# Performance work log

Measured on AMD Instinct MI355X. Metric: run time of the kernel, lower is better.

## Reference

```python
import jax, jax.numpy as jnp
import numpy as np

NUM_HEADS = 8
NUM_LAYERS = 4
ATTN_DIM = 256
INPUT_DIM = 256
HEAD_DIM = ATTN_DIM // NUM_HEADS


def setup_inputs() -> dict:
    key = jax.random.key(0)
    ks = jax.random.split(key, 4)
    B, N = 32, 512
    agents_state = jax.random.normal(ks[0], (B, N, INPUT_DIM), dtype=jnp.float32)
    # normc_initializer(0.01): small std weights; bias zeros (torch default bias is
    # uniform but zeros suffice for a baseline; kept as explicit params)
    Wq = jax.random.normal(ks[1], (ATTN_DIM, INPUT_DIM), dtype=jnp.float32) * 0.01
    Wk = jax.random.normal(ks[2], (ATTN_DIM, INPUT_DIM), dtype=jnp.float32) * 0.01
    Wv = jax.random.normal(ks[3], (ATTN_DIM, INPUT_DIM), dtype=jnp.float32) * 0.01
    bq = jnp.zeros((ATTN_DIM,), dtype=jnp.float32)
    bk = jnp.zeros((ATTN_DIM,), dtype=jnp.float32)
    bv = jnp.zeros((ATTN_DIM,), dtype=jnp.float32)
    return {"agents_state": agents_state, "Wq": Wq, "bq": bq, "Wk": Wk, "bk": bk, "Wv": Wv, "bv": bv}


def _mha(q, k, v):
    # q: [B, N, D]; k, v: [B, M, D]
    B, N, _ = q.shape
    M = k.shape[1]
    qh = q.reshape(B, N, NUM_HEADS, HEAD_DIM)
    kh = k.reshape(B, M, NUM_HEADS, HEAD_DIM)
    vh = v.reshape(B, M, NUM_HEADS, HEAD_DIM)
    scores = jnp.einsum('bnhd,bmhd->bnhm', qh, kh) / np.float32(HEAD_DIM ** 0.5)
    attn = jax.nn.softmax(scores, axis=-1)
    out = jnp.einsum('bnhm,bmhd->bnhd', attn, vh)
    return out.reshape(B, N, ATTN_DIM)


def reference(agents_state, Wq, bq, Wk, bk, Wv, bv):
    queries = agents_state @ Wq.T + bq
    keys = agents_state @ Wk.T + bk
    values = agents_state @ Wv.T + bv
    attn_output = queries
    for _ in range(NUM_LAYERS):
        attn_output = attn_output + _mha(attn_output, keys, values)
    return attn_output
```

## Files before the change

kernel.cpp:

```cpp
#include <hip/hip_runtime.h>

typedef __bf16 bf16x8 __attribute__((ext_vector_type(8)));
typedef float  f32x4  __attribute__((ext_vector_type(4)));

#define K_SCALE 0.25505402682247326f

static __device__ __forceinline__ unsigned short f2bf(float f) {
  return __builtin_bit_cast(unsigned short, (__bf16)f);
}
static __device__ __forceinline__ f32x4 mfma16(bf16x8 a, bf16x8 b, f32x4 c) {
  return __builtin_amdgcn_mfma_f32_16x16x32_bf16(a, b, c, 0, 0, 0);
}

__global__ __launch_bounds__(256) void prep_kernel(
    const float* __restrict__ Wq, const float* __restrict__ bq,
    const float* __restrict__ Wk, const float* __restrict__ bk,
    const float* __restrict__ Wv, const float* __restrict__ bv,
    unsigned short* __restrict__ Wf, float* __restrict__ bias) {
  if (blockIdx.x == 96) {
    int t = threadIdx.x;
#pragma unroll
    for (int kseg = 0; kseg < 3; ++kseg) {
      int i = kseg * 256 + t;
      float bb;
      if (i < 256)      bb = bq[i];
      else if (i < 512) bb = bk[i - 256] * K_SCALE;
      else              bb = bv[i - 512];
      bias[i] = bb;
    }
    return;
  }
  int fidx = blockIdx.x * 256 + threadIdx.x;
  int lane = fidx & 63;
  int ks = (fidx >> 6) & 7;
  int ct = fidx >> 9;
  int n = ct * 16 + (lane & 15);
  int kk = ks * 32 + (lane >> 4) * 8;
  const float* src;
  float scale = 1.0f;
  if (n < 256)      src = Wq + n * 256 + kk;
  else if (n < 512) { src = Wk + (n - 256) * 256 + kk; scale = K_SCALE; }
  else              src = Wv + (n - 512) * 256 + kk;
  float4 f0 = reinterpret_cast<const float4*>(src)[0];
  float4 f1 = reinterpret_cast<const float4*>(src)[1];
  bf16x8 h;
  h[0] = (__bf16)(f0.x * scale); h[1] = (__bf16)(f0.y * scale);
  h[2] = (__bf16)(f0.z * scale); h[3] = (__bf16)(f0.w * scale);
  h[4] = (__bf16)(f1.x * scale); h[5] = (__bf16)(f1.y * scale);
  h[6] = (__bf16)(f1.z * scale); h[7] = (__bf16)(f1.w * scale);
  *reinterpret_cast<bf16x8*>(Wf + fidx * 8) = h;
}

__global__ __launch_bounds__(512, 4) void qkv_kernel(
    const float* __restrict__ X, const unsigned short* __restrict__ Wf,
    const float* __restrict__ bias, float* __restrict__ Qout,
    unsigned short* __restrict__ Kb, unsigned short* __restrict__ Vt) {
  __shared__ __align__(16) unsigned short Alds[32 * 256];
  const int tid = threadIdx.x;
  const int rowbase = blockIdx.x * 32;
  {
    int idx = tid * 16;
    int r = idx >> 8, k = idx & 255;
    const float4* src = reinterpret_cast<const float4*>(X + (rowbase + r) * 256 + k);
    float4 f0 = src[0], f1 = src[1], f2 = src[2], f3 = src[3];
    bf16x8 h0, h1;
    h0[0]=(__bf16)f0.x; h0[1]=(__bf16)f0.y; h0[2]=(__bf16)f0.z; h0[3]=(__bf16)f0.w;
    h0[4]=(__bf16)f1.x; h0[5]=(__bf16)f1.y; h0[6]=(__bf16)f1.z; h0[7]=(__bf16)f1.w;
    h1[0]=(__bf16)f2.x; h1[1]=(__bf16)f2.y; h1[2]=(__bf16)f2.z; h1[3]=(__bf16)f2.w;
    h1[4]=(__bf16)f3.x; h1[5]=(__bf16)f3.y; h1[6]=(__bf16)f3.z; h1[7]=(__bf16)f3.w;
    int c0 = k >> 3;
    int p0 = (c0 & 24) | ((c0 ^ r) & 7);
    int p1 = ((c0 + 1) & 24) | (((c0 + 1) ^ r) & 7);
    *reinterpret_cast<bf16x8*>(&Alds[r * 256 + p0 * 8]) = h0;
    *reinterpret_cast<bf16x8*>(&Alds[r * 256 + p1 * 8]) = h1;
  }
  __syncthreads();
  const int w = tid >> 6, lane = tid & 63, c = lane & 15, quad = lane >> 4;
  const f32x4 zf = {0.f, 0.f, 0.f, 0.f};
  for (int p = 0; p < 6; ++p) {
    int ct = w * 6 + p;
    f32x4 acc[2] = {zf, zf};
#pragma unroll
    for (int ks = 0; ks < 8; ++ks) {
      bf16x8 bf = *reinterpret_cast<const bf16x8*>(Wf + ((ct * 8 + ks) * 64 + lane) * 8);
#pragma unroll
      for (int mg = 0; mg < 2; ++mg) {
        int m = mg * 16 + c;
        int c8 = ks * 4 + quad;
        int ph = (c8 & 24) | ((c8 ^ m) & 7);
        bf16x8 af = *reinterpret_cast<const bf16x8*>(&Alds[m * 256 + ph * 8]);
        acc[mg] = mfma16(af, bf, acc[mg]);
      }
    }
    int col = ct * 16 + c;
    float bb = bias[col];
#pragma unroll
    for (int mg = 0; mg < 2; ++mg) {
      int growb = rowbase + mg * 16 + quad * 4;
      int b = growb >> 9, nrow = growb & 511;
      if (col < 256) {
#pragma unroll
        for (int r = 0; r < 4; ++r)
          Qout[(growb + r) * 256 + col] = acc[mg][r] + bb;
      } else if (col < 512) {
        int d = col & 31, hh = (col - 256) >> 5;
        int pd = ((d >> 2) & 3) * 8 + ((d >> 4) & 1) * 4 + (d & 3);
#pragma unroll
        for (int r = 0; r < 4; ++r)
          Kb[((b * 8 + hh) * 512 + nrow + r) * 32 + pd] = f2bf(acc[mg][r] + bb);
      } else {
        int d = col & 31, hh = (col - 512) >> 5;
        int pnb = (nrow & ~31) + ((nrow >> 2) & 3) * 8 + ((nrow >> 4) & 1) * 4;
        ushort4 pk;
        pk.x = f2bf(acc[mg][0] + bb); pk.y = f2bf(acc[mg][1] + bb);
        pk.z = f2bf(acc[mg][2] + bb); pk.w = f2bf(acc[mg][3] + bb);
        *reinterpret_cast<ushort4*>(&Vt[((b * 8 + hh) * 32 + d) * 512 + pnb]) = pk;
      }
    }
  }
}

__global__ __launch_bounds__(512, 4) void attn_kernel(
    const float* Q0, const unsigned short* __restrict__ Kg,
    const unsigned short* __restrict__ Vg, float* Out) {
  __shared__ __align__(16) unsigned short Ks[16384];
  __shared__ __align__(16) unsigned short Vts[16384];
  const int tid = threadIdx.x;
  const int bh = blockIdx.x >> 1, seg = blockIdx.x & 1;
  const int b = bh >> 3, h = bh & 7;
  const unsigned short* kgp = Kg + bh * 16384;
  const unsigned short* vgp = Vg + bh * 16384;
#pragma unroll
  for (int it = 0; it < 4; ++it) {
    int idx = it * 4096 + tid * 8;
    {
      int n = idx >> 5, g = (idx >> 3) & 3;
      bf16x8 v = *reinterpret_cast<const bf16x8*>(kgp + idx);
      *reinterpret_cast<bf16x8*>(&Ks[n * 32 + ((g ^ ((n >> 1) & 3)) << 3)]) = v;
    }
    {
      int d = idx >> 9, nn = idx & 511;
      bf16x8 v = *reinterpret_cast<const bf16x8*>(vgp + idx);
      int g = (nn >> 3) ^ (d & 7);
      *reinterpret_cast<bf16x8*>(&Vts[d * 512 + g * 8]) = v;
    }
  }
  const int w = tid >> 6, lane = tid & 63, c = lane & 15, quad = lane >> 4;
  const int rowq = seg * 256 + w * 32;
  f32x4 x[2][2];
#pragma unroll
  for (int rg = 0; rg < 2; ++rg)
#pragma unroll
    for (int tt = 0; tt < 2; ++tt)
      x[rg][tt] = *reinterpret_cast<const f32x4*>(
          Q0 + (b * 512 + rowq + rg * 16 + c) * 256 + h * 32 + tt * 16 + quad * 4);
  __syncthreads();
  const f32x4 zf = {0.f, 0.f, 0.f, 0.f};
  bf16x8 ones;
#pragma unroll
  for (int j = 0; j < 8; ++j) ones[j] = (__bf16)1.0f;
#pragma unroll 1
  for (int layer = 0; layer < 4; ++layer) {
    bf16x8 aq[2];
#pragma unroll
    for (int rg = 0; rg < 2; ++rg) {
      aq[rg][0] = (__bf16)x[rg][0][0]; aq[rg][1] = (__bf16)x[rg][0][1];
      aq[rg][2] = (__bf16)x[rg][0][2]; aq[rg][3] = (__bf16)x[rg][0][3];
      aq[rg][4] = (__bf16)x[rg][1][0]; aq[rg][5] = (__bf16)x[rg][1][1];
      aq[rg][6] = (__bf16)x[rg][1][2]; aq[rg][7] = (__bf16)x[rg][1][3];
    }
    f32x4 sacc[2] = {zf, zf};
    f32x4 O[2][2] = {{zf, zf}, {zf, zf}};
#pragma unroll 4
    for (int ch = 0; ch < 16; ++ch) {
      f32x4 S[2][2];
#pragma unroll
      for (int tt = 0; tt < 2; ++tt) {
        int n = (ch * 2 + tt) * 16 + c;
        bf16x8 kf = *reinterpret_cast<const bf16x8*>(
            &Ks[n * 32 + ((quad ^ ((c >> 1) & 3)) << 3)]);
#pragma unroll
        for (int rg = 0; rg < 2; ++rg) S[rg][tt] = mfma16(kf, aq[rg], zf);
      }
      bf16x8 ap[2];
#pragma unroll
      for (int rg = 0; rg < 2; ++rg) {
#pragma unroll
        for (int tt = 0; tt < 2; ++tt)
#pragma unroll
          for (int r = 0; r < 4; ++r)
            S[rg][tt][r] = __builtin_amdgcn_exp2f(S[rg][tt][r]);
        ap[rg][0] = (__bf16)S[rg][0][0]; ap[rg][1] = (__bf16)S[rg][0][1];
        ap[rg][2] = (__bf16)S[rg][0][2]; ap[rg][3] = (__bf16)S[rg][0][3];
        ap[rg][4] = (__bf16)S[rg][1][0]; ap[rg][5] = (__bf16)S[rg][1][1];
        ap[rg][6] = (__bf16)S[rg][1][2]; ap[rg][7] = (__bf16)S[rg][1][3];
        sacc[rg] = mfma16(ones, ap[rg], sacc[rg]);
      }
#pragma unroll
      for (int tt = 0; tt < 2; ++tt) {
        int d = tt * 16 + c;
        int gv = (ch * 4 + quad) ^ (c & 7);
        bf16x8 vf = *reinterpret_cast<const bf16x8*>(&Vts[d * 512 + gv * 8]);
#pragma unroll
        for (int rg = 0; rg < 2; ++rg) O[rg][tt] = mfma16(vf, ap[rg], O[rg][tt]);
      }
    }
#pragma unroll
    for (int rg = 0; rg < 2; ++rg) {
      float inv = __builtin_amdgcn_rcpf(sacc[rg][0]);
#pragma unroll
      for (int tt = 0; tt < 2; ++tt)
#pragma unroll
        for (int r = 0; r < 4; ++r) x[rg][tt][r] += O[rg][tt][r] * inv;
    }
  }
#pragma unroll
  for (int rg = 0; rg < 2; ++rg)
#pragma unroll
    for (int tt = 0; tt < 2; ++tt)
      *reinterpret_cast<f32x4*>(
          Out + (b * 512 + rowq + rg * 16 + c) * 256 + h * 32 + tt * 16 + quad * 4) = x[rg][tt];
}

extern "C" void kernel_launch(void* const* d_in, const int* in_sizes, int n_in,
                              void* d_out, int out_size, void* d_ws, size_t ws_size,
                              hipStream_t stream) {
  const float* X  = (const float*)d_in[0];
  const float* Wq = (const float*)d_in[1];
  const float* bq = (const float*)d_in[2];
  const float* Wk = (const float*)d_in[3];
  const float* bk = (const float*)d_in[4];
  const float* Wv = (const float*)d_in[5];
  const float* bv = (const float*)d_in[6];
  char* ws = (char*)d_ws;
  unsigned short* Wf   = (unsigned short*)(ws);
  float*          bias = (float*)(ws + 393216);
  unsigned short* Kb   = (unsigned short*)(ws + 397312);
  unsigned short* Vt   = (unsigned short*)(ws + 397312 + 8388608);
  float* out = (float*)d_out;
  prep_kernel<<<97, 256, 0, stream>>>(Wq, bq, Wk, bk, Wv, bv, Wf, bias);
  qkv_kernel<<<512, 512, 0, stream>>>(X, Wf, bias, out, Kb, Vt);
  attn_kernel<<<512, 512, 0, stream>>>(out, Kb, Vt, out);
}
```

Measured before the change: 132.8 us.

## Read K/V fragments directly from global memory instead of staging in LDS

The attention kernel no longer copies each head's K and V into shared memory. Each wave now loads its MFMA operand fragments straight from global memory (served by L1/L2), and the V output layout in the QKV kernel is changed so that each lane's fragment is a contiguous 16-byte load. Blocks shrink to 256 threads and the grid doubles to 1024, ordered so that both halves of a head are spread across the grid. This removes the LDS fill, the barrier and the LDS footprint, which should raise occupancy, but it makes every K/V read hit the cache hierarchy repeatedly across layers and waves.

Measured after the change: 142.2 us. +7.0%, slower.

```diff
diff --git a/kernel.cpp b/kernel.cpp
--- a/kernel.cpp
+++ b/kernel.cpp
@@ -110,43 +110,28 @@
           Kb[((b * 8 + hh) * 512 + nrow + r) * 32 + pd] = f2bf(acc[mg][r] + bb);
       } else {
         int d = col & 31, hh = (col - 512) >> 5;
-        int pnb = (nrow & ~31) + ((nrow >> 2) & 3) * 8 + ((nrow >> 4) & 1) * 4;
+        int tt = d >> 4, m = d & 15;
+        int ch = nrow >> 5, qq = (nrow >> 2) & 3, jb = ((nrow >> 4) & 1) * 4;
         ushort4 pk;
         pk.x = f2bf(acc[mg][0] + bb); pk.y = f2bf(acc[mg][1] + bb);
         pk.z = f2bf(acc[mg][2] + bb); pk.w = f2bf(acc[mg][3] + bb);
-        *reinterpret_cast<ushort4*>(&Vt[((b * 8 + hh) * 32 + d) * 512 + pnb]) = pk;
+        *reinterpret_cast<ushort4*>(
+            &Vt[(((b * 8 + hh) * 16 + ch) * 2 + tt) * 512 + (qq * 16 + m) * 8 + jb]) = pk;
       }
     }
   }
 }
 
-__global__ __launch_bounds__(512, 4) void attn_kernel(
+__global__ __launch_bounds__(256, 4) void attn_kernel(
     const float* Q0, const unsigned short* __restrict__ Kg,
     const unsigned short* __restrict__ Vg, float* Out) {
-  __shared__ __align__(16) unsigned short Ks[16384];
-  __shared__ __align__(16) unsigned short Vts[16384];
   const int tid = threadIdx.x;
-  const int bh = blockIdx.x >> 1, seg = blockIdx.x & 1;
+  const int bh = blockIdx.x & 255, seg = blockIdx.x >> 8;
   const int b = bh >> 3, h = bh & 7;
   const unsigned short* kgp = Kg + bh * 16384;
   const unsigned short* vgp = Vg + bh * 16384;
-#pragma unroll
-  for (int it = 0; it < 4; ++it) {
-    int idx = it * 4096 + tid * 8;
-    {
-      int n = idx >> 5, g = (idx >> 3) & 3;
-      bf16x8 v = *reinterpret_cast<const bf16x8*>(kgp + idx);
-      *reinterpret_cast<bf16x8*>(&Ks[n * 32 + ((g ^ ((n >> 1) & 3)) << 3)]) = v;
-    }
-    {
-      int d = idx >> 9, nn = idx & 511;
-      bf16x8 v = *reinterpret_cast<const bf16x8*>(vgp + idx);
-      int g = (nn >> 3) ^ (d & 7);
-      *reinterpret_cast<bf16x8*>(&Vts[d * 512 + g * 8]) = v;
-    }
-  }
   const int w = tid >> 6, lane = tid & 63, c = lane & 15, quad = lane >> 4;
-  const int rowq = seg * 256 + w * 32;
+  const int rowq = seg * 128 + w * 32;
   f32x4 x[2][2];
 #pragma unroll
   for (int rg = 0; rg < 2; ++rg)
@@ -154,7 +139,6 @@
     for (int tt = 0; tt < 2; ++tt)
       x[rg][tt] = *reinterpret_cast<const f32x4*>(
           Q0 + (b * 512 + rowq + rg * 16 + c) * 256 + h * 32 + tt * 16 + quad * 4);
-  __syncthreads();
   const f32x4 zf = {0.f, 0.f, 0.f, 0.f};
   bf16x8 ones;
 #pragma unroll
@@ -173,15 +157,21 @@
     f32x4 O[2][2] = {{zf, zf}, {zf, zf}};
 #pragma unroll 4
     for (int ch = 0; ch < 16; ++ch) {
+      bf16x8 kf[2];
+#pragma unroll
+      for (int tt = 0; tt < 2; ++tt)
+        kf[tt] = *reinterpret_cast<const bf16x8*>(
+            kgp + ((ch * 2 + tt) * 16 + c) * 32 + quad * 8);
       f32x4 S[2][2];
 #pragma unroll
-      for (int tt = 0; tt < 2; ++tt) {
-        int n = (ch * 2 + tt) * 16 + c;
-        bf16x8 kf = *reinterpret_cast<const bf16x8*>(
-            &Ks[n * 32 + ((quad ^ ((c >> 1) & 3)) << 3)]);
-#pragma unroll
-        for (int rg = 0; rg < 2; ++rg) S[rg][tt] = mfma16(kf, aq[rg], zf);
-      }
+      for (int tt = 0; tt < 2; ++tt)
+#pragma unroll
+        for (int rg = 0; rg < 2; ++rg) S[rg][tt] = mfma16(kf[tt], aq[rg], zf);
+      bf16x8 vf[2];
+#pragma unroll
+      for (int tt = 0; tt < 2; ++tt)
+        vf[tt] = *reinterpret_cast<const bf16x8*>(
+            vgp + ((ch * 2 + tt) * 64 + lane) * 8);
       bf16x8 ap[2];
 #pragma unroll
       for (int rg = 0; rg < 2; ++rg) {
@@ -197,13 +187,9 @@
         sacc[rg] = mfma16(ones, ap[rg], sacc[rg]);
       }
 #pragma unroll
-      for (int tt = 0; tt < 2; ++tt) {
-        int d = tt * 16 + c;
-        int gv = (ch * 4 + quad) ^ (c & 7);
-        bf16x8 vf = *reinterpret_cast<const bf16x8*>(&Vts[d * 512 + gv * 8]);
-#pragma unroll
-        for (int rg = 0; rg < 2; ++rg) O[rg][tt] = mfma16(vf, ap[rg], O[rg][tt]);
-      }
+      for (int tt = 0; tt < 2; ++tt)
+#pragma unroll
+        for (int rg = 0; rg < 2; ++rg) O[rg][tt] = mfma16(vf[tt], ap[rg], O[rg][tt]);
     }
 #pragma unroll
     for (int rg = 0; rg < 2; ++rg) {
@@ -240,5 +226,5 @@
   float* out = (float*)d_out;
   prep_kernel<<<97, 256, 0, stream>>>(Wq, bq, Wk, bk, Wv, bv, Wf, bias);
   qkv_kernel<<<512, 512, 0, stream>>>(X, Wf, bias, out, Kb, Vt);
-  attn_kernel<<<512, 512, 0, stream>>>(out, Kb, Vt, out);
-}
+  attn_kernel<<<1024, 256, 0, stream>>>(out, Kb, Vt, out);
+}
```

## Fuse QKV projection into attention kernel, computing per-head K/V directly into LDS

Applied to the files above, without the earlier changes.

Removes the separate QKV GEMM kernel and the global K/V/Q round-trip. The prep kernel now also converts X to bf16, and each attention block computes its head's K and V projections straight into shared memory in MFMA-friendly layouts, plus its own Q rows in registers. The cost is that K/V for each (batch, head) are computed twice, once by each of the two sequence-segment blocks. The block also does extra GEMM work before the attention loop and reads bf16 X from global memory.

Result: slower. 153.2 us (+15.4%).

```diff
diff --git a/kernel.cpp b/kernel.cpp
--- a/kernel.cpp
+++ b/kernel.cpp
@@ -13,11 +13,27 @@
 }
 
 __global__ __launch_bounds__(256) void prep_kernel(
+    const float* __restrict__ X,
     const float* __restrict__ Wq, const float* __restrict__ bq,
     const float* __restrict__ Wk, const float* __restrict__ bk,
     const float* __restrict__ Wv, const float* __restrict__ bv,
-    unsigned short* __restrict__ Wf, float* __restrict__ bias) {
-  if (blockIdx.x == 96) {
+    unsigned short* __restrict__ Xb, unsigned short* __restrict__ Wf,
+    float* __restrict__ bias) {
+  int blk = blockIdx.x;
+  if (blk < 1024) {
+    int idx = blk * 4096 + threadIdx.x * 16;
+    const float4* src = reinterpret_cast<const float4*>(X + idx);
+    float4 f0 = src[0], f1 = src[1], f2 = src[2], f3 = src[3];
+    bf16x8 h0, h1;
+    h0[0]=(__bf16)f0.x; h0[1]=(__bf16)f0.y; h0[2]=(__bf16)f0.z; h0[3]=(__bf16)f0.w;
+    h0[4]=(__bf16)f1.x; h0[5]=(__bf16)f1.y; h0[6]=(__bf16)f1.z; h0[7]=(__bf16)f1.w;
+    h1[0]=(__bf16)f2.x; h1[1]=(__bf16)f2.y; h1[2]=(__bf16)f2.z; h1[3]=(__bf16)f2.w;
+    h1[4]=(__bf16)f3.x; h1[5]=(__bf16)f3.y; h1[6]=(__bf16)f3.z; h1[7]=(__bf16)f3.w;
+    *reinterpret_cast<bf16x8*>(Xb + idx) = h0;
+    *reinterpret_cast<bf16x8*>(Xb + idx + 8) = h1;
+    return;
+  }
+  if (blk == 1120) {
     int t = threadIdx.x;
 #pragma unroll
     for (int kseg = 0; kseg < 3; ++kseg) {
@@ -30,7 +46,7 @@
     }
     return;
   }
-  int fidx = blockIdx.x * 256 + threadIdx.x;
+  int fidx = (blk - 1024) * 256 + threadIdx.x;
   int lane = fidx & 63;
   int ks = (fidx >> 6) & 7;
   int ct = fidx >> 9;
@@ -51,111 +67,99 @@
   *reinterpret_cast<bf16x8*>(Wf + fidx * 8) = h;
 }
 
-__global__ __launch_bounds__(512, 4) void qkv_kernel(
-    const float* __restrict__ X, const unsigned short* __restrict__ Wf,
-    const float* __restrict__ bias, float* __restrict__ Qout,
-    unsigned short* __restrict__ Kb, unsigned short* __restrict__ Vt) {
-  __shared__ __align__(16) unsigned short Alds[32 * 256];
-  const int tid = threadIdx.x;
-  const int rowbase = blockIdx.x * 32;
-  {
-    int idx = tid * 16;
-    int r = idx >> 8, k = idx & 255;
-    const float4* src = reinterpret_cast<const float4*>(X + (rowbase + r) * 256 + k);
-    float4 f0 = src[0], f1 = src[1], f2 = src[2], f3 = src[3];
-    bf16x8 h0, h1;
-    h0[0]=(__bf16)f0.x; h0[1]=(__bf16)f0.y; h0[2]=(__bf16)f0.z; h0[3]=(__bf16)f0.w;
-    h0[4]=(__bf16)f1.x; h0[5]=(__bf16)f1.y; h0[6]=(__bf16)f1.z; h0[7]=(__bf16)f1.w;
-    h1[0]=(__bf16)f2.x; h1[1]=(__bf16)f2.y; h1[2]=(__bf16)f2.z; h1[3]=(__bf16)f2.w;
-    h1[4]=(__bf16)f3.x; h1[5]=(__bf16)f3.y; h1[6]=(__bf16)f3.z; h1[7]=(__bf16)f3.w;
-    int c0 = k >> 3;
-    int p0 = (c0 & 24) | ((c0 ^ r) & 7);
-    int p1 = ((c0 + 1) & 24) | (((c0 + 1) ^ r) & 7);
-    *reinterpret_cast<bf16x8*>(&Alds[r * 256 + p0 * 8]) = h0;
-    *reinterpret_cast<bf16x8*>(&Alds[r * 256 + p1 * 8]) = h1;
-  }
-  __syncthreads();
-  const int w = tid >> 6, lane = tid & 63, c = lane & 15, quad = lane >> 4;
-  const f32x4 zf = {0.f, 0.f, 0.f, 0.f};
-  for (int p = 0; p < 6; ++p) {
-    int ct = w * 6 + p;
-    f32x4 acc[2] = {zf, zf};
-#pragma unroll
-    for (int ks = 0; ks < 8; ++ks) {
-      bf16x8 bf = *reinterpret_cast<const bf16x8*>(Wf + ((ct * 8 + ks) * 64 + lane) * 8);
-#pragma unroll
-      for (int mg = 0; mg < 2; ++mg) {
-        int m = mg * 16 + c;
-        int c8 = ks * 4 + quad;
-        int ph = (c8 & 24) | ((c8 ^ m) & 7);
-        bf16x8 af = *reinterpret_cast<const bf16x8*>(&Alds[m * 256 + ph * 8]);
-        acc[mg] = mfma16(af, bf, acc[mg]);
-      }
-    }
-    int col = ct * 16 + c;
-    float bb = bias[col];
-#pragma unroll
-    for (int mg = 0; mg < 2; ++mg) {
-      int growb = rowbase + mg * 16 + quad * 4;
-      int b = growb >> 9, nrow = growb & 511;
-      if (col < 256) {
-#pragma unroll
-        for (int r = 0; r < 4; ++r)
-          Qout[(growb + r) * 256 + col] = acc[mg][r] + bb;
-      } else if (col < 512) {
-        int d = col & 31, hh = (col - 256) >> 5;
-        int pd = ((d >> 2) & 3) * 8 + ((d >> 4) & 1) * 4 + (d & 3);
-#pragma unroll
-        for (int r = 0; r < 4; ++r)
-          Kb[((b * 8 + hh) * 512 + nrow + r) * 32 + pd] = f2bf(acc[mg][r] + bb);
-      } else {
-        int d = col & 31, hh = (col - 512) >> 5;
-        int pnb = (nrow & ~31) + ((nrow >> 2) & 3) * 8 + ((nrow >> 4) & 1) * 4;
-        ushort4 pk;
-        pk.x = f2bf(acc[mg][0] + bb); pk.y = f2bf(acc[mg][1] + bb);
-        pk.z = f2bf(acc[mg][2] + bb); pk.w = f2bf(acc[mg][3] + bb);
-        *reinterpret_cast<ushort4*>(&Vt[((b * 8 + hh) * 32 + d) * 512 + pnb]) = pk;
-      }
-    }
-  }
-}
-
 __global__ __launch_bounds__(512, 4) void attn_kernel(
-    const float* Q0, const unsigned short* __restrict__ Kg,
-    const unsigned short* __restrict__ Vg, float* Out) {
+    const unsigned short* __restrict__ Xb, const unsigned short* __restrict__ Wf,
+    const float* __restrict__ bias, float* __restrict__ Out) {
   __shared__ __align__(16) unsigned short Ks[16384];
-  __shared__ __align__(16) unsigned short Vts[16384];
+  __shared__ __align__(16) unsigned short Vf[16384];
   const int tid = threadIdx.x;
   const int bh = blockIdx.x >> 1, seg = blockIdx.x & 1;
   const int b = bh >> 3, h = bh & 7;
-  const unsigned short* kgp = Kg + bh * 16384;
-  const unsigned short* vgp = Vg + bh * 16384;
-#pragma unroll
-  for (int it = 0; it < 4; ++it) {
-    int idx = it * 4096 + tid * 8;
-    {
-      int n = idx >> 5, g = (idx >> 3) & 3;
-      bf16x8 v = *reinterpret_cast<const bf16x8*>(kgp + idx);
-      *reinterpret_cast<bf16x8*>(&Ks[n * 32 + ((g ^ ((n >> 1) & 3)) << 3)]) = v;
-    }
-    {
-      int d = idx >> 9, nn = idx & 511;
-      bf16x8 v = *reinterpret_cast<const bf16x8*>(vgp + idx);
-      int g = (nn >> 3) ^ (d & 7);
-      *reinterpret_cast<bf16x8*>(&Vts[d * 512 + g * 8]) = v;
-    }
-  }
   const int w = tid >> 6, lane = tid & 63, c = lane & 15, quad = lane >> 4;
+  const f32x4 zf = {0.f, 0.f, 0.f, 0.f};
+  const int kw = w * 64;
+  f32x4 accK[2][4], accV[4][2];
+#pragma unroll
+  for (int dt = 0; dt < 2; ++dt)
+#pragma unroll
+    for (int kt = 0; kt < 4; ++kt) { accK[dt][kt] = zf; accV[kt][dt] = zf; }
+#pragma unroll
+  for (int ks = 0; ks < 8; ++ks) {
+    bf16x8 bX[4];
+#pragma unroll
+    for (int kt = 0; kt < 4; ++kt)
+      bX[kt] = *reinterpret_cast<const bf16x8*>(
+          Xb + (b * 512 + kw + kt * 16 + c) * 256 + ks * 32 + quad * 8);
+    bf16x8 aWk[2], aWv[2];
+#pragma unroll
+    for (int dt = 0; dt < 2; ++dt) {
+      aWk[dt] = *reinterpret_cast<const bf16x8*>(
+          Wf + (((16 + h * 2 + dt) * 8 + ks) * 64 + lane) * 8);
+      aWv[dt] = *reinterpret_cast<const bf16x8*>(
+          Wf + (((32 + h * 2 + dt) * 8 + ks) * 64 + lane) * 8);
+    }
+#pragma unroll
+    for (int dt = 0; dt < 2; ++dt)
+#pragma unroll
+      for (int kt = 0; kt < 4; ++kt)
+        accK[dt][kt] = mfma16(aWk[dt], bX[kt], accK[dt][kt]);
+#pragma unroll
+    for (int mt = 0; mt < 4; ++mt)
+#pragma unroll
+      for (int nt = 0; nt < 2; ++nt)
+        accV[mt][nt] = mfma16(bX[mt], aWv[nt], accV[mt][nt]);
+  }
+#pragma unroll
+  for (int dt = 0; dt < 2; ++dt) {
+    f32x4 bk4 = *reinterpret_cast<const f32x4*>(bias + 256 + h * 32 + dt * 16 + quad * 4);
+#pragma unroll
+    for (int kt = 0; kt < 4; ++kt) {
+      int n = kw + kt * 16 + c;
+      int slot = quad ^ ((n >> 1) & 3);
+      ushort4 pk;
+      pk.x = f2bf(accK[dt][kt][0] + bk4[0]); pk.y = f2bf(accK[dt][kt][1] + bk4[1]);
+      pk.z = f2bf(accK[dt][kt][2] + bk4[2]); pk.w = f2bf(accK[dt][kt][3] + bk4[3]);
+      *reinterpret_cast<ushort4*>(&Ks[n * 32 + slot * 8 + dt * 4]) = pk;
+    }
+  }
+#pragma unroll
+  for (int nt = 0; nt < 2; ++nt) {
+    float bv1 = bias[512 + h * 32 + nt * 16 + c];
+#pragma unroll
+    for (int mt = 0; mt < 4; ++mt) {
+      ushort4 pk;
+      pk.x = f2bf(accV[mt][nt][0] + bv1); pk.y = f2bf(accV[mt][nt][1] + bv1);
+      pk.z = f2bf(accV[mt][nt][2] + bv1); pk.w = f2bf(accV[mt][nt][3] + bv1);
+      *reinterpret_cast<ushort4*>(
+          &Vf[((w * 2 + (mt >> 1)) * 2 + nt) * 512 + (quad * 16 + c) * 8 + (mt & 1) * 4]) = pk;
+    }
+  }
   const int rowq = seg * 256 + w * 32;
-  f32x4 x[2][2];
-#pragma unroll
-  for (int rg = 0; rg < 2; ++rg)
+  f32x4 x[2][2] = {{zf, zf}, {zf, zf}};
+#pragma unroll
+  for (int ks = 0; ks < 8; ++ks) {
+    bf16x8 bXq[2], aQ[2];
+#pragma unroll
+    for (int rg = 0; rg < 2; ++rg)
+      bXq[rg] = *reinterpret_cast<const bf16x8*>(
+          Xb + (b * 512 + rowq + rg * 16 + c) * 256 + ks * 32 + quad * 8);
 #pragma unroll
     for (int tt = 0; tt < 2; ++tt)
-      x[rg][tt] = *reinterpret_cast<const f32x4*>(
-          Q0 + (b * 512 + rowq + rg * 16 + c) * 256 + h * 32 + tt * 16 + quad * 4);
+      aQ[tt] = *reinterpret_cast<const bf16x8*>(
+          Wf + (((h * 2 + tt) * 8 + ks) * 64 + lane) * 8);
+#pragma unroll
+    for (int rg = 0; rg < 2; ++rg)
+#pragma unroll
+      for (int tt = 0; tt < 2; ++tt)
+        x[rg][tt] = mfma16(aQ[tt], bXq[rg], x[rg][tt]);
+  }
+#pragma unroll
+  for (int tt = 0; tt < 2; ++tt) {
+    f32x4 bq4 = *reinterpret_cast<const f32x4*>(bias + h * 32 + tt * 16 + quad * 4);
+#pragma unroll
+    for (int rg = 0; rg < 2; ++rg) x[rg][tt] += bq4;
+  }
   __syncthreads();
-  const f32x4 zf = {0.f, 0.f, 0.f, 0.f};
   bf16x8 ones;
 #pragma unroll
   for (int j = 0; j < 8; ++j) ones[j] = (__bf16)1.0f;
@@ -178,7 +182,7 @@
       for (int tt = 0; tt < 2; ++tt) {
         int n = (ch * 2 + tt) * 16 + c;
         bf16x8 kf = *reinterpret_cast<const bf16x8*>(
-            &Ks[n * 32 + ((quad ^ ((c >> 1) & 3)) << 3)]);
+            &Ks[n * 32 + ((quad ^ ((n >> 1) & 3)) << 3)]);
 #pragma unroll
         for (int rg = 0; rg < 2; ++rg) S[rg][tt] = mfma16(kf, aq[rg], zf);
       }
@@ -198,9 +202,8 @@
       }
 #pragma unroll
       for (int tt = 0; tt < 2; ++tt) {
-        int d = tt * 16 + c;
-        int gv = (ch * 4 + quad) ^ (c & 7);
-        bf16x8 vf = *reinterpret_cast<const bf16x8*>(&Vts[d * 512 + gv * 8]);
+        bf16x8 vf = *reinterpret_cast<const bf16x8*>(
+            &Vf[((ch * 2 + tt) * 64 + lane) * 8]);
 #pragma unroll
         for (int rg = 0; rg < 2; ++rg) O[rg][tt] = mfma16(vf, ap[rg], O[rg][tt]);
       }
@@ -235,10 +238,8 @@
   char* ws = (char*)d_ws;
   unsigned short* Wf   = (unsigned short*)(ws);
   float*          bias = (float*)(ws + 393216);
-  unsigned short* Kb   = (unsigned short*)(ws + 397312);
-  unsigned short* Vt   = (unsigned short*)(ws + 397312 + 8388608);
+  unsigned short* Xb   = (unsigned short*)(ws + 397312);
   float* out = (float*)d_out;
-  prep_kernel<<<97, 256, 0, stream>>>(Wq, bq, Wk, bk, Wv, bv, Wf, bias);
-  qkv_kernel<<<512, 512, 0, stream>>>(X, Wf, bias, out, Kb, Vt);
-  attn_kernel<<<512, 512, 0, stream>>>(out, Kb, Vt, out);
-}
+  prep_kernel<<<1121, 256, 0, stream>>>(X, Wq, bq, Wk, bk, Wv, bv, Xb, Wf, bias);
+  attn_kernel<<<512, 512, 0, stream>>>(Xb, Wf, bias, out);
+}
```
